# Performance work log

Hardware: AMD Instinct MI355X
Metric: run time of the kernel (lower is better)

## Reference

```python
import jax, jax.numpy as jnp
import numpy as np

N_NODES = 50000
N_EDGES = 800000
D_IN = 128
D_OUT = 128


def setup_inputs() -> dict:
    key = jax.random.key(0)
    k1, k2, k3, k4, k5 = jax.random.split(key, 5)
    x = jax.random.normal(k1, (N_NODES, D_IN), dtype=jnp.float32)
    # fc weight, torch Linear convention: [out_dim, in_dim]
    W = jax.random.normal(k2, (D_OUT, D_IN), dtype=jnp.float32) * (1.0 / np.sqrt(D_IN))
    # attn_fc weight: [1, 2*out_dim], no bias
    a = jax.random.normal(k3, (1, 2 * D_OUT), dtype=jnp.float32) * (1.0 / np.sqrt(2 * D_OUT))
    src = jax.random.randint(k4, (N_EDGES,), 0, N_NODES)
    dst = jax.random.randint(k5, (N_EDGES,), 0, N_NODES)
    return {"x": x, "W": W, "a": a, "src": src, "dst": dst}


def reference(x, W, a, src, dst):
    # h = fc(x)
    h = x @ W.T  # [N, D_OUT]
    # attn_fc(cat([h_src, h_dst])) == h_src @ a[:D] + h_dst @ a[D:] (linear, no bias),
    # so precompute per-node scalars instead of materializing [E, 2*D_OUT].
    a_src = a[0, :D_OUT]
    a_dst = a[0, D_OUT:]
    s = h @ a_src  # [N]
    d = h @ a_dst  # [N]
    e = jax.nn.sigmoid(s[src] + d[dst])[:, None]  # [E, 1]
    msg = e * h[src]  # [E, D_OUT]  edge gather + weight
    # reduce: f[v] = sum over incoming edges of e * h_src
    f = jax.ops.segment_sum(msg, dst, num_segments=N_NODES)  # [N, D_OUT]
    return f
```

## Files before the change

kernel.cpp:

```cpp
#include <hip/hip_runtime.h>
#include <hip/hip_bf16.h>
#include <stdint.h>

#define NN 50000
#define NE 800000
#define DD 128
#define NBKT 782
#define BCH 4096
#define BGRID ((NE + BCH - 1) / BCH)
#define CAP 1280
#define SPILL_CAP 32768
#define GROWS 32
#define GGRID ((NN + GROWS - 1) / GROWS)

typedef __attribute__((ext_vector_type(8))) unsigned short ushort8;
typedef __attribute__((ext_vector_type(8))) short short8;
typedef __attribute__((ext_vector_type(4))) float f32x4;

__device__ inline uint16_t f2bf(float f) {
    uint32_t u = __float_as_uint(f);
    return (uint16_t)((u + 0x7fffu + ((u >> 16) & 1u)) >> 16);
}
__device__ inline float bf_lo(uint32_t u) { return __uint_as_float(u << 16); }
__device__ inline float bf_hi(uint32_t u) { return __uint_as_float(u & 0xffff0000u); }

__global__ __launch_bounds__(256) void wconv_k(const float* __restrict__ W,
                                               uint16_t* __restrict__ Wb,
                                               int* __restrict__ cntg) {
    int t = threadIdx.x;
    if (blockIdx.x == 0) {
        for (int k = t; k < NBKT + 4; k += 256) cntg[k] = 0;
    }
    int i = blockIdx.x * 256 + t;
    if (i < DD * DD) Wb[i] = f2bf(W[i]);
}

__global__ __launch_bounds__(256) void gemm_mfma_k(const float* __restrict__ x,
                                                   const uint16_t* __restrict__ Wb,
                                                   const float* __restrict__ a,
                                                   uint16_t* __restrict__ hb,
                                                   float* __restrict__ sArr,
                                                   float* __restrict__ dArr) {
    __shared__ __align__(16) uint16_t hs[GROWS][136];
    __shared__ float sdl[2 * GROWS];
    const int t = threadIdx.x, l = t & 63, wid = t >> 6;
    const int r0 = blockIdx.x * GROWS;
    const int wr0 = (wid >> 1) * 16;
    const int wc0 = (wid & 1) * 64;
    const int lr = l & 15, lk = l >> 4;
    if (t < 2 * GROWS) sdl[t] = 0.f;
    __syncthreads();

    f32x4 acc[4] = {{0.f,0.f,0.f,0.f},{0.f,0.f,0.f,0.f},{0.f,0.f,0.f,0.f},{0.f,0.f,0.f,0.f}};
    const int arow = r0 + wr0 + lr;
    const bool rok = arow < NN;
    const float* xp = x + (size_t)arow * DD + lk * 8;

    #pragma unroll
    for (int kc = 0; kc < 4; ++kc) {
        short8 af;
        if (rok) {
            float4 v0 = *(const float4*)(xp + kc * 32);
            float4 v1 = *(const float4*)(xp + kc * 32 + 4);
            af[0] = (short)f2bf(v0.x); af[1] = (short)f2bf(v0.y);
            af[2] = (short)f2bf(v0.z); af[3] = (short)f2bf(v0.w);
            af[4] = (short)f2bf(v1.x); af[5] = (short)f2bf(v1.y);
            af[6] = (short)f2bf(v1.z); af[7] = (short)f2bf(v1.w);
        } else {
            af = short8{0,0,0,0,0,0,0,0};
        }
        #pragma unroll
        for (int c = 0; c < 4; ++c) {
            int col = wc0 + c * 16 + lr;
            short8 bf_ = *(const short8*)(Wb + (size_t)col * DD + kc * 32 + lk * 8);
            acc[c] = __builtin_amdgcn_mfma_f32_16x16x32_bf16(af, bf_, acc[c], 0, 0, 0);
        }
    }

    float avs[4], avd[4];
    #pragma unroll
    for (int c = 0; c < 4; ++c) {
        avs[c] = a[wc0 + c * 16 + lr];
        avd[c] = a[DD + wc0 + c * 16 + lr];
    }
    #pragma unroll
    for (int i = 0; i < 4; ++i) {
        float ps = 0.f, pd = 0.f;
        #pragma unroll
        for (int c = 0; c < 4; ++c) {
            ps = fmaf(acc[c][i], avs[c], ps);
            pd = fmaf(acc[c][i], avd[c], pd);
        }
        #pragma unroll
        for (int o = 8; o > 0; o >>= 1) {
            ps += __shfl_xor(ps, o);
            pd += __shfl_xor(pd, o);
        }
        if (lr == 0) {
            int brow = wr0 + lk * 4 + i;
            atomicAdd(&sdl[brow], ps);
            atomicAdd(&sdl[GROWS + brow], pd);
        }
    }
    #pragma unroll
    for (int c = 0; c < 4; ++c)
        #pragma unroll
        for (int i = 0; i < 4; ++i)
            hs[wr0 + lk * 4 + i][wc0 + c * 16 + lr] = f2bf(acc[c][i]);
    __syncthreads();

    {
        int row = t >> 3, colg = (t & 7) * 16;
        int grow = r0 + row;
        if (grow < NN) {
            ushort8 v0 = *(const ushort8*)&hs[row][colg];
            ushort8 v1 = *(const ushort8*)&hs[row][colg + 8];
            *(ushort8*)(hb + (size_t)grow * DD + colg) = v0;
            *(ushort8*)(hb + (size_t)grow * DD + colg + 8) = v1;
        }
    }
    if (t < GROWS) {
        int grow = r0 + t;
        if (grow < NN) { sArr[grow] = sdl[t]; dArr[grow] = sdl[GROWS + t]; }
    }
}

__global__ __launch_bounds__(256) void bscat_k(const int* __restrict__ src,
                                               const int* __restrict__ dst,
                                               const float* __restrict__ sA,
                                               const float* __restrict__ dA,
                                               int* __restrict__ cntg,
                                               int* __restrict__ spill_cnt,
                                               uint2* __restrict__ rec,
                                               uint4* __restrict__ spill) {
    __shared__ int lh[NBKT];
    __shared__ int gb[NBKT];
    int t = threadIdx.x;
    for (int k = t; k < NBKT; k += 256) lh[k] = 0;
    __syncthreads();
    int base = blockIdx.x * BCH;
    unsigned pk[16]; int bk[16]; float ev[16];
    #pragma unroll
    for (int i = 0; i < 16; ++i) {
        int idx = base + i * 256 + t;
        if (idx < NE) {
            int s_ = src[idx], d_ = dst[idx];
            bk[i] = d_ >> 6;
            pk[i] = ((unsigned)(d_ & 63) << 16) | (unsigned)s_;
            float z = sA[s_] + dA[d_];
            ev[i] = 1.f / (1.f + __expf(-z));
            atomicAdd(&lh[bk[i]], 1);
        } else bk[i] = -1;
    }
    __syncthreads();
    for (int k = t; k < NBKT; k += 256) {
        int c = lh[k];
        lh[k] = 0;
        if (c) gb[k] = atomicAdd(&cntg[k], c);
    }
    __syncthreads();
    #pragma unroll
    for (int i = 0; i < 16; ++i) {
        if (bk[i] >= 0) {
            int sl = atomicAdd(&lh[bk[i]], 1);
            int p = gb[bk[i]] + sl;
            if (p < CAP) {
                rec[(size_t)bk[i] * CAP + p] = make_uint2(pk[i], __float_as_uint(ev[i]));
            } else {
                int sp = atomicAdd(spill_cnt, 1);
                if (sp < SPILL_CAP)
                    spill[sp] = make_uint4(pk[i] & 0xffffu,
                                           (unsigned)(bk[i] * 64 + (int)(pk[i] >> 16)),
                                           __float_as_uint(ev[i]), 0u);
            }
        }
    }
}

__global__ __launch_bounds__(512) void bsort_agg_k(const uint32_t* __restrict__ hb,
                                                   const int* __restrict__ cntg,
                                                   const uint2* __restrict__ rec,
                                                   float* __restrict__ out) {
    __shared__ uint2 srt[CAP];
    __shared__ int h64[64];
    __shared__ int s65[65];
    __shared__ int curw[64];
    int t = threadIdx.x, l = t & 63, wid = t >> 6;
    int b = blockIdx.x;
    int cnt = cntg[b]; if (cnt > CAP) cnt = CAP;
    int beg = b * CAP;
    int n0 = b * 64;
    if (t < 64) h64[t] = 0;
    __syncthreads();

    for (int j = t; j < cnt; j += 512) {
        uint2 r = rec[beg + j];
        atomicAdd(&h64[r.x >> 16], 1);
    }
    __syncthreads();
    if (wid == 0) {
        int v = h64[l];
        int inc = v;
        #pragma unroll
        for (int o = 1; o < 64; o <<= 1) {
            int nb = __shfl_up(inc, o);
            if (l >= o) inc += nb;
        }
        s65[l + 1] = inc;
        if (l == 0) s65[0] = 0;
        curw[l] = inc - v;
    }
    __syncthreads();
    for (int j = t; j < cnt; j += 512) {
        uint2 r = rec[beg + j];
        int p = atomicAdd(&curw[r.x >> 16], 1);
        srt[p] = r;
    }
    __syncthreads();
    #pragma unroll 1
    for (int rr = 0; rr < 8; ++rr) {
        int d = wid * 8 + rr;
        int n = n0 + d;
        if (n >= NN) break;
        int js = s65[d], je = s65[d + 1];
        float2 a0 = {0.f,0.f}, a1 = {0.f,0.f}, a2 = {0.f,0.f}, a3 = {0.f,0.f};
        int j = js;
        for (; j + 3 < je; j += 4) {
            uint2 r0 = srt[j], r1 = srt[j+1], r2 = srt[j+2], r3 = srt[j+3];
            uint32_t u0 = hb[(size_t)(r0.x & 0xffffu) * 64 + l];
            uint32_t u1 = hb[(size_t)(r1.x & 0xffffu) * 64 + l];
            uint32_t u2 = hb[(size_t)(r2.x & 0xffffu) * 64 + l];
            uint32_t u3 = hb[(size_t)(r3.x & 0xffffu) * 64 + l];
            float e0 = __uint_as_float(r0.y), e1 = __uint_as_float(r1.y);
            float e2 = __uint_as_float(r2.y), e3 = __uint_as_float(r3.y);
            a0.x = fmaf(e0, bf_lo(u0), a0.x); a0.y = fmaf(e0, bf_hi(u0), a0.y);
            a1.x = fmaf(e1, bf_lo(u1), a1.x); a1.y = fmaf(e1, bf_hi(u1), a1.y);
            a2.x = fmaf(e2, bf_lo(u2), a2.x); a2.y = fmaf(e2, bf_hi(u2), a2.y);
            a3.x = fmaf(e3, bf_lo(u3), a3.x); a3.y = fmaf(e3, bf_hi(u3), a3.y);
        }
        for (; j < je; ++j) {
            uint2 r0 = srt[j];
            uint32_t u0 = hb[(size_t)(r0.x & 0xffffu) * 64 + l];
            float e0 = __uint_as_float(r0.y);
            a0.x = fmaf(e0, bf_lo(u0), a0.x); a0.y = fmaf(e0, bf_hi(u0), a0.y);
        }
        float2 res;
        res.x = (a0.x + a1.x) + (a2.x + a3.x);
        res.y = (a0.y + a1.y) + (a2.y + a3.y);
        ((float2*)out)[(size_t)n * 64 + l] = res;
    }
}

__global__ __launch_bounds__(256) void spill_k(const int* __restrict__ spill_cnt,
                                               const uint4* __restrict__ spill,
                                               const uint32_t* __restrict__ hb,
                                               float* __restrict__ out) {
    int n = *spill_cnt; if (n > SPILL_CAP) n = SPILL_CAP;
    int w = blockIdx.x * 4 + (threadIdx.x >> 6), l = threadIdx.x & 63;
    for (int i = w; i < n; i += 32) {
        uint4 r = spill[i];
        uint32_t u = hb[(size_t)r.x * 64 + l];
        float e = __uint_as_float(r.z);
        atomicAdd(&out[(size_t)r.y * DD + 2 * l],     e * bf_lo(u));
        atomicAdd(&out[(size_t)r.y * DD + 2 * l + 1], e * bf_hi(u));
    }
}

__global__ __launch_bounds__(256) void edge_atomic_k(const int* __restrict__ src, const int* __restrict__ dst,
                                                     const float* __restrict__ sArr, const float* __restrict__ dArr,
                                                     const uint32_t* __restrict__ hb, float* __restrict__ out) {
    int wid = threadIdx.x >> 6, l = threadIdx.x & 63;
    int e = blockIdx.x * 4 + wid;
    if (e >= NE) return;
    int sv = src[e], dv = dst[e];
    float z = sArr[sv] + dArr[dv];
    float ev = 1.0f / (1.0f + __expf(-z));
    uint32_t u = hb[(size_t)sv * 64 + l];
    atomicAdd(&out[(size_t)dv * DD + 2 * l],     ev * bf_lo(u));
    atomicAdd(&out[(size_t)dv * DD + 2 * l + 1], ev * bf_hi(u));
}

extern "C" void kernel_launch(void* const* d_in, const int* in_sizes, int n_in,
                              void* d_out, int out_size, void* d_ws, size_t ws_size,
                              hipStream_t stream) {
    const float* x  = (const float*)d_in[0];
    const float* W  = (const float*)d_in[1];
    const float* a  = (const float*)d_in[2];
    const int* src  = (const int*)d_in[3];
    const int* dst  = (const int*)d_in[4];
    float* out = (float*)d_out;

    char* p = (char*)d_ws;
    uint16_t* hb = (uint16_t*)p;            p += (size_t)NN * DD * 2;
    uint16_t* Wb = (uint16_t*)p;            p += (size_t)DD * DD * 2;
    float* sA    = (float*)p;               p += (size_t)NN * 4;
    float* dA    = (float*)p;               p += (size_t)NN * 4;
    int*   cntg  = (int*)p;                 p += (size_t)NBKT * 4;
    int*   scnt  = (int*)p;                 p += 16;
    uint2* rec   = (uint2*)(((uintptr_t)p + 15) & ~(uintptr_t)15);
    p = (char*)(rec + (size_t)NBKT * CAP);
    uint4* spill = (uint4*)p;               p += (size_t)SPILL_CAP * 16;
    size_t need  = (size_t)(p - (char*)d_ws);

    if (ws_size >= need) {
        wconv_k<<<64, 256, 0, stream>>>(W, Wb, cntg);
        gemm_mfma_k<<<GGRID, 256, 0, stream>>>(x, Wb, a, hb, sA, dA);
        bscat_k<<<BGRID, 256, 0, stream>>>(src, dst, sA, dA, cntg, scnt, rec, spill);
        bsort_agg_k<<<NBKT, 512, 0, stream>>>((const uint32_t*)hb, cntg, rec, out);
        spill_k<<<8, 256, 0, stream>>>(scnt, spill, (const uint32_t*)hb, out);
    } else {
        hipMemsetAsync(out, 0, sizeof(float) * (size_t)NN * DD, stream);
        wconv_k<<<64, 256, 0, stream>>>(W, Wb, cntg);
        gemm_mfma_k<<<GGRID, 256, 0, stream>>>(x, Wb, a, hb, sA, dA);
        edge_atomic_k<<<NE / 4, 256, 0, stream>>>(src, dst, sA, dA, (const uint32_t*)hb, out);
    }
}
```

Before: 88.05 us.

## Defer edge sigmoid to aggregation kernel and shrink bucket records to 4 bytes

The edge weight sigmoid(sA[src]+dA[dst]) is no longer computed in the scatter kernel and stored with each record. It is now computed in the sort/aggregate kernel, using dA values staged in shared memory for the bucket's 64 destination nodes. This halves the record size written and read through global memory and removes the random dA gathers from the scatter pass. In exchange, records are cached in registers (up to 3 per thread) between the histogram and placement passes, and the aggregate kernel takes on the random sA gathers and the exp work.

```diff
diff --git a/kernel.cpp b/kernel.cpp
--- a/kernel.cpp
+++ b/kernel.cpp
@@ -127,19 +127,17 @@
 
 __global__ __launch_bounds__(256) void bscat_k(const int* __restrict__ src,
                                                const int* __restrict__ dst,
-                                               const float* __restrict__ sA,
-                                               const float* __restrict__ dA,
                                                int* __restrict__ cntg,
                                                int* __restrict__ spill_cnt,
-                                               uint2* __restrict__ rec,
-                                               uint4* __restrict__ spill) {
+                                               uint32_t* __restrict__ rec,
+                                               uint2* __restrict__ spill) {
     __shared__ int lh[NBKT];
     __shared__ int gb[NBKT];
     int t = threadIdx.x;
     for (int k = t; k < NBKT; k += 256) lh[k] = 0;
     __syncthreads();
     int base = blockIdx.x * BCH;
-    unsigned pk[16]; int bk[16]; float ev[16];
+    unsigned pk[16]; int bk[16];
     #pragma unroll
     for (int i = 0; i < 16; ++i) {
         int idx = base + i * 256 + t;
@@ -147,8 +145,6 @@
             int s_ = src[idx], d_ = dst[idx];
             bk[i] = d_ >> 6;
             pk[i] = ((unsigned)(d_ & 63) << 16) | (unsigned)s_;
-            float z = sA[s_] + dA[d_];
-            ev[i] = 1.f / (1.f + __expf(-z));
             atomicAdd(&lh[bk[i]], 1);
         } else bk[i] = -1;
     }
@@ -165,23 +161,26 @@
             int sl = atomicAdd(&lh[bk[i]], 1);
             int p = gb[bk[i]] + sl;
             if (p < CAP) {
-                rec[(size_t)bk[i] * CAP + p] = make_uint2(pk[i], __float_as_uint(ev[i]));
+                rec[(size_t)bk[i] * CAP + p] = pk[i];
             } else {
                 int sp = atomicAdd(spill_cnt, 1);
                 if (sp < SPILL_CAP)
-                    spill[sp] = make_uint4(pk[i] & 0xffffu,
-                                           (unsigned)(bk[i] * 64 + (int)(pk[i] >> 16)),
-                                           __float_as_uint(ev[i]), 0u);
+                    spill[sp] = make_uint2(pk[i] & 0xffffu,
+                                           (unsigned)(bk[i] * 64 + (int)(pk[i] >> 16)));
             }
         }
     }
 }
 
 __global__ __launch_bounds__(512) void bsort_agg_k(const uint32_t* __restrict__ hb,
+                                                   const float* __restrict__ sA,
+                                                   const float* __restrict__ dA,
                                                    const int* __restrict__ cntg,
-                                                   const uint2* __restrict__ rec,
+                                                   const uint32_t* __restrict__ rec,
                                                    float* __restrict__ out) {
-    __shared__ uint2 srt[CAP];
+    __shared__ uint32_t srt[CAP];
+    __shared__ float    eL[CAP];
+    __shared__ float dAl[64];
     __shared__ int h64[64];
     __shared__ int s65[65];
     __shared__ int curw[64];
@@ -190,12 +189,18 @@
     int cnt = cntg[b]; if (cnt > CAP) cnt = CAP;
     int beg = b * CAP;
     int n0 = b * 64;
-    if (t < 64) h64[t] = 0;
-    __syncthreads();
-
+    if (t < 64) {
+        h64[t] = 0;
+        int n = n0 + t;
+        dAl[t] = (n < NN) ? dA[n] : 0.f;
+    }
+    __syncthreads();
+
+    uint32_t rc[3]; int nrc = 0;
     for (int j = t; j < cnt; j += 512) {
-        uint2 r = rec[beg + j];
-        atomicAdd(&h64[r.x >> 16], 1);
+        uint32_t r = rec[beg + j];
+        rc[nrc++] = r;
+        atomicAdd(&h64[r >> 16], 1);
     }
     __syncthreads();
     if (wid == 0) {
@@ -211,10 +216,13 @@
         curw[l] = inc - v;
     }
     __syncthreads();
-    for (int j = t; j < cnt; j += 512) {
-        uint2 r = rec[beg + j];
-        int p = atomicAdd(&curw[r.x >> 16], 1);
+    for (int k = 0; k < nrc; ++k) {
+        uint32_t r = rc[k];
+        int d = (int)(r >> 16);
+        int p = atomicAdd(&curw[d], 1);
+        float z = sA[r & 0xffffu] + dAl[d];
         srt[p] = r;
+        eL[p] = 1.f / (1.f + __expf(-z));
     }
     __syncthreads();
     #pragma unroll 1
@@ -226,22 +234,21 @@
         float2 a0 = {0.f,0.f}, a1 = {0.f,0.f}, a2 = {0.f,0.f}, a3 = {0.f,0.f};
         int j = js;
         for (; j + 3 < je; j += 4) {
-            uint2 r0 = srt[j], r1 = srt[j+1], r2 = srt[j+2], r3 = srt[j+3];
-            uint32_t u0 = hb[(size_t)(r0.x & 0xffffu) * 64 + l];
-            uint32_t u1 = hb[(size_t)(r1.x & 0xffffu) * 64 + l];
-            uint32_t u2 = hb[(size_t)(r2.x & 0xffffu) * 64 + l];
-            uint32_t u3 = hb[(size_t)(r3.x & 0xffffu) * 64 + l];
-            float e0 = __uint_as_float(r0.y), e1 = __uint_as_float(r1.y);
-            float e2 = __uint_as_float(r2.y), e3 = __uint_as_float(r3.y);
+            uint32_t r0 = srt[j], r1 = srt[j+1], r2 = srt[j+2], r3 = srt[j+3];
+            float e0 = eL[j], e1 = eL[j+1], e2 = eL[j+2], e3 = eL[j+3];
+            uint32_t u0 = hb[(size_t)(r0 & 0xffffu) * 64 + l];
+            uint32_t u1 = hb[(size_t)(r1 & 0xffffu) * 64 + l];
+            uint32_t u2 = hb[(size_t)(r2 & 0xffffu) * 64 + l];
+            uint32_t u3 = hb[(size_t)(r3 & 0xffffu) * 64 + l];
             a0.x = fmaf(e0, bf_lo(u0), a0.x); a0.y = fmaf(e0, bf_hi(u0), a0.y);
             a1.x = fmaf(e1, bf_lo(u1), a1.x); a1.y = fmaf(e1, bf_hi(u1), a1.y);
             a2.x = fmaf(e2, bf_lo(u2), a2.x); a2.y = fmaf(e2, bf_hi(u2), a2.y);
             a3.x = fmaf(e3, bf_lo(u3), a3.x); a3.y = fmaf(e3, bf_hi(u3), a3.y);
         }
         for (; j < je; ++j) {
-            uint2 r0 = srt[j];
-            uint32_t u0 = hb[(size_t)(r0.x & 0xffffu) * 64 + l];
-            float e0 = __uint_as_float(r0.y);
+            uint32_t r0 = srt[j];
+            float e0 = eL[j];
+            uint32_t u0 = hb[(size_t)(r0 & 0xffffu) * 64 + l];
             a0.x = fmaf(e0, bf_lo(u0), a0.x); a0.y = fmaf(e0, bf_hi(u0), a0.y);
         }
         float2 res;
@@ -252,15 +259,18 @@
 }
 
 __global__ __launch_bounds__(256) void spill_k(const int* __restrict__ spill_cnt,
-                                               const uint4* __restrict__ spill,
+                                               const uint2* __restrict__ spill,
+                                               const float* __restrict__ sA,
+                                               const float* __restrict__ dA,
                                                const uint32_t* __restrict__ hb,
                                                float* __restrict__ out) {
     int n = *spill_cnt; if (n > SPILL_CAP) n = SPILL_CAP;
     int w = blockIdx.x * 4 + (threadIdx.x >> 6), l = threadIdx.x & 63;
     for (int i = w; i < n; i += 32) {
-        uint4 r = spill[i];
+        uint2 r = spill[i];
+        float z = sA[r.x] + dA[r.y];
+        float e = 1.f / (1.f + __expf(-z));
         uint32_t u = hb[(size_t)r.x * 64 + l];
-        float e = __uint_as_float(r.z);
         atomicAdd(&out[(size_t)r.y * DD + 2 * l],     e * bf_lo(u));
         atomicAdd(&out[(size_t)r.y * DD + 2 * l + 1], e * bf_hi(u));
     }
@@ -297,17 +307,17 @@
     float* dA    = (float*)p;               p += (size_t)NN * 4;
     int*   cntg  = (int*)p;                 p += (size_t)NBKT * 4;
     int*   scnt  = (int*)p;                 p += 16;
-    uint2* rec   = (uint2*)(((uintptr_t)p + 15) & ~(uintptr_t)15);
+    uint32_t* rec = (uint32_t*)(((uintptr_t)p + 15) & ~(uintptr_t)15);
     p = (char*)(rec + (size_t)NBKT * CAP);
-    uint4* spill = (uint4*)p;               p += (size_t)SPILL_CAP * 16;
+    uint2* spill = (uint2*)p;               p += (size_t)SPILL_CAP * 8;
     size_t need  = (size_t)(p - (char*)d_ws);
 
     if (ws_size >= need) {
         wconv_k<<<64, 256, 0, stream>>>(W, Wb, cntg);
         gemm_mfma_k<<<GGRID, 256, 0, stream>>>(x, Wb, a, hb, sA, dA);
-        bscat_k<<<BGRID, 256, 0, stream>>>(src, dst, sA, dA, cntg, scnt, rec, spill);
-        bsort_agg_k<<<NBKT, 512, 0, stream>>>((const uint32_t*)hb, cntg, rec, out);
-        spill_k<<<8, 256, 0, stream>>>(scnt, spill, (const uint32_t*)hb, out);
+        bscat_k<<<BGRID, 256, 0, stream>>>(src, dst, cntg, scnt, rec, spill);
+        bsort_agg_k<<<NBKT, 512, 0, stream>>>((const uint32_t*)hb, sA, dA, cntg, rec, out);
+        spill_k<<<8, 256, 0, stream>>>(scnt, spill, sA, dA, (const uint32_t*)hb, out);
     } else {
         hipMemsetAsync(out, 0, sizeof(float) * (size_t)NN * DD, stream);
         wconv_k<<<64, 256, 0, stream>>>(W, Wb, cntg);
```

After: 85.92 us. 2.4% less time.
